# Optimization experiments

Hardware: AMD Instinct MI355X
Metric: run time of the kernel (lower is better)

Reference implementation:

```python
import jax, jax.numpy as jnp
import numpy as np

N_POINTS = 50000   # rows of features, also number of output segments
N_EDGES = 1600000  # ragged neighborhood edges (out_idx, in_idx)
CHANNELS = 64


def setup_inputs() -> dict:
    key = jax.random.key(0)
    k1, k2 = jax.random.split(key)
    features = jax.random.normal(k1, (N_POINTS, CHANNELS), dtype=jnp.float32)
    sparse_indices = jax.random.randint(
        k2, (N_EDGES, 2), 0, N_POINTS, dtype=jnp.int64
    )
    return {"features": features, "sparse_indices": sparse_indices}


def reference(features, sparse_indices):
    # sparse_indices[:, 0] = output segment id, sparse_indices[:, 1] = input row.
    out_idx = sparse_indices[:, 0]
    in_idx = sparse_indices[:, 1]
    gathered = features[in_idx]  # [E, C] gather of neighbor features
    # Unsorted segment max over the ragged neighborhoods -> [N, C].
    pooled = jax.ops.segment_max(gathered, out_idx, num_segments=N_POINTS)
    return pooled
```

## Files before the change

### kernel.cpp

```cpp
#include <hip/hip_runtime.h>
#include <hip/hip_bf16.h>
#include <math.h>


#define N_POINTS 50000
#define N_EDGES  1600000
#define CHANNELS 64
#define BIN_SHIFT 7
#define BIN_PTS   128
#define NBINS     391
#define NBINS_PAD 512
#define CAPB      5120
#define QCAP      1536
#define ECHUNK    4096
#define N_P1_BLOCKS ((N_EDGES + ECHUNK - 1) / ECHUNK)
#define GCUR_STRIDE 16
#define CVT_TOTAL (N_POINTS * CHANNELS / 4)
#define CVT_PER   2047

__device__ __forceinline__ unsigned int encode_bf16(float x) {
    unsigned int u = __float_as_uint(x);
    unsigned int r = ((u >> 16) & 1u) + 0x7FFFu;
    unsigned int h = (u + r) >> 16;
    return (h & 0x8000u) ? (h ^ 0xFFFFu) : (h | 0x8000u);
}

__device__ __forceinline__ float decode_u16(unsigned int v) {
    if (v == 0u) return -INFINITY;
    unsigned int h = (v & 0x8000u) ? (v ^ 0x8000u) : (v ^ 0xFFFFu);
    return __uint_as_float(h << 16);
}

__global__ __launch_bounds__(512) void binsort_cvt_kernel(
    const int2*   __restrict__ idx,
    const float4* __restrict__ feat4,
    uint2*        __restrict__ f16o,
    unsigned int* __restrict__ gcur,
    unsigned int* __restrict__ gstage)
{
    __shared__ unsigned int hist[NBINS_PAD];
    __shared__ unsigned int pfx[NBINS_PAD];
    __shared__ unsigned int gbase[NBINS_PAD];
    __shared__ unsigned int staging[ECHUNK];
    __shared__ unsigned int wsum[8];

    int tid  = threadIdx.x;
    int lane = tid & 63, w = tid >> 6;

    {
        int base = blockIdx.x * CVT_PER;
        #pragma unroll
        for (int k = 0; k < 4; ++k) {
            int i = base + k * 512 + tid;
            if (i < base + CVT_PER && i < CVT_TOTAL) {
                float4 v = feat4[i];
                uint2 r;
                r.x = encode_bf16(v.x) | (encode_bf16(v.y) << 16);
                r.y = encode_bf16(v.z) | (encode_bf16(v.w) << 16);
                f16o[i] = r;
            }
        }
    }

    int base = blockIdx.x * ECHUNK;
    int cnt  = N_EDGES - base; if (cnt > ECHUNK) cnt = ECHUNK;

    if (tid < NBINS_PAD) hist[tid] = 0u;
    __syncthreads();

    int2 e[8]; unsigned int slot[8];
    #pragma unroll
    for (int j = 0; j < 8; ++j) {
        int i = j * 512 + tid;
        if (i < cnt) {
            e[j] = idx[base + i];
            slot[j] = atomicAdd(&hist[(unsigned)e[j].x >> BIN_SHIFT], 1u);
        }
    }
    __syncthreads();

    unsigned int a = (tid < NBINS_PAD) ? hist[tid] : 0u;
    unsigned int inc = a;
    #pragma unroll
    for (int d = 1; d < 64; d <<= 1) {
        unsigned int v = __shfl_up(inc, d, 64);
        if (lane >= d) inc += v;
    }
    if (lane == 63) wsum[w] = inc;
    __syncthreads();
    unsigned int woff = 0;
    #pragma unroll
    for (int k = 0; k < 8; ++k) if (k < w) woff += wsum[k];
    if (tid < NBINS_PAD) {
        pfx[tid] = woff + inc - a;
        if (a) gbase[tid] = atomicAdd(&gcur[tid * GCUR_STRIDE], a);
    }
    __syncthreads();

    #pragma unroll
    for (int j = 0; j < 8; ++j) {
        int i = j * 512 + tid;
        if (i < cnt) {
            unsigned int dst = (unsigned)e[j].x, src = (unsigned)e[j].y;
            unsigned int bin = dst >> BIN_SHIFT;
            staging[pfx[bin] + slot[j]] =
                (bin << 23) | ((dst & (BIN_PTS - 1)) << 16) | src;
        }
    }
    __syncthreads();

    for (int i = tid; i < cnt; i += 512) {
        unsigned int v   = staging[i];
        unsigned int bin = v >> 23;
        unsigned int g   = gbase[bin] + ((unsigned)i - pfx[bin]);
        if (g < CAPB) gstage[(size_t)bin * CAPB + g] = v;
    }
}

__global__ __launch_bounds__(256) void pool_kernel(
    const unsigned int* __restrict__ feat16,
    const unsigned int* __restrict__ gcur,
    const unsigned int* __restrict__ gstage,
    float2* __restrict__ out2)
{
    __shared__ unsigned int sorted[QCAP];
    __shared__ unsigned int hist[32];
    __shared__ unsigned int start[33];
    __shared__ unsigned int cur[32];

    int tid = threadIdx.x;
    int bin = blockIdx.x >> 2;
    int quarter = blockIdx.x & 3;

    unsigned int cnt = gcur[bin * GCUR_STRIDE]; if (cnt > CAPB) cnt = CAPB;
    const uint4* list4 = (const uint4*)(gstage + (size_t)bin * CAPB);

    if (tid < 32) hist[tid] = 0u;
    __syncthreads();

    unsigned int e[16]; int ne = 0;
    for (unsigned int b4 = tid; b4 * 4 < cnt; b4 += 256) {
        uint4 v = list4[b4];
        unsigned int bi = b4 * 4;
        unsigned int vv[4] = {v.x, v.y, v.z, v.w};
        #pragma unroll
        for (int k = 0; k < 4; ++k) {
            if (bi + k < cnt) {
                unsigned int dl = (vv[k] >> 16) & (BIN_PTS - 1);
                if ((int)(dl >> 5) == quarter) {
                    e[ne++] = vv[k];
                    atomicAdd(&hist[dl & 31], 1u);
                }
            }
        }
    }
    __syncthreads();

    if (tid < 32) {
        unsigned int h = hist[tid], inc = h;
        #pragma unroll
        for (int d = 1; d < 32; d <<= 1) {
            unsigned int v = __shfl_up(inc, d, 64);
            if (tid >= d) inc += v;
        }
        start[tid] = inc - h; cur[tid] = inc - h;
        if (tid == 31) start[32] = inc;
    }
    __syncthreads();

    for (int j = 0; j < ne; ++j) {
        unsigned int v = e[j];
        unsigned int slot = atomicAdd(&cur[(v >> 16) & 31], 1u);
        if (slot < QCAP) sorted[slot] = v;
    }
    __syncthreads();

    int hw = tid >> 5, c2 = tid & 31;
    for (int p = hw; p < 32; p += 8) {
        unsigned int s0 = start[p], s1 = start[p + 1];
        if (s1 > QCAP) s1 = QCAP;
        unsigned int A0=0,A1=0,B0=0,B1=0,C0=0,C1=0,D0=0,D1=0;
        unsigned int E0=0,E1=0,F0=0,F1=0,G0=0,G1=0,H0=0,H1=0;
        unsigned int i = s0;
        for (; i + 8 <= s1; i += 8) {
            unsigned int u0 = feat16[(sorted[i+0] & 0xFFFFu) * 32 + c2];
            unsigned int u1 = feat16[(sorted[i+1] & 0xFFFFu) * 32 + c2];
            unsigned int u2 = feat16[(sorted[i+2] & 0xFFFFu) * 32 + c2];
            unsigned int u3 = feat16[(sorted[i+3] & 0xFFFFu) * 32 + c2];
            unsigned int u4 = feat16[(sorted[i+4] & 0xFFFFu) * 32 + c2];
            unsigned int u5 = feat16[(sorted[i+5] & 0xFFFFu) * 32 + c2];
            unsigned int u6 = feat16[(sorted[i+6] & 0xFFFFu) * 32 + c2];
            unsigned int u7 = feat16[(sorted[i+7] & 0xFFFFu) * 32 + c2];
            A0 = max(A0, u0 & 0xFFFFu); A1 = max(A1, u0 >> 16);
            B0 = max(B0, u1 & 0xFFFFu); B1 = max(B1, u1 >> 16);
            C0 = max(C0, u2 & 0xFFFFu); C1 = max(C1, u2 >> 16);
            D0 = max(D0, u3 & 0xFFFFu); D1 = max(D1, u3 >> 16);
            E0 = max(E0, u4 & 0xFFFFu); E1 = max(E1, u4 >> 16);
            F0 = max(F0, u5 & 0xFFFFu); F1 = max(F1, u5 >> 16);
            G0 = max(G0, u6 & 0xFFFFu); G1 = max(G1, u6 >> 16);
            H0 = max(H0, u7 & 0xFFFFu); H1 = max(H1, u7 >> 16);
        }
        for (; i < s1; ++i) {
            unsigned int u = feat16[(sorted[i] & 0xFFFFu) * 32 + c2];
            A0 = max(A0, u & 0xFFFFu); A1 = max(A1, u >> 16);
        }
        A0 = max(max(max(A0,B0), max(C0,D0)), max(max(E0,F0), max(G0,H0)));
        A1 = max(max(max(A1,B1), max(C1,D1)), max(max(E1,F1), max(G1,H1)));

        int gp = bin * BIN_PTS + quarter * 32 + p;
        if (gp < N_POINTS) {
            float2 f; f.x = decode_u16(A0); f.y = decode_u16(A1);
            out2[(size_t)gp * 32 + c2] = f;
        }
    }
}

extern "C" void kernel_launch(void* const* d_in, const int* in_sizes, int n_in,
                              void* d_out, int out_size, void* d_ws, size_t ws_size,
                              hipStream_t stream) {
    const float4* feat4 = (const float4*)d_in[0];
    const int2*   idx   = (const int2*)d_in[1];

    size_t off_gcur   = 0;
    size_t off_feat16 = (size_t)NBINS_PAD * GCUR_STRIDE * 4;
    size_t off_gstage = off_feat16 + (size_t)N_POINTS * CHANNELS * 2;
    unsigned int* gcur   = (unsigned int*)((char*)d_ws + off_gcur);
    uint2*        f16o   = (uint2*)((char*)d_ws + off_feat16);
    unsigned int* feat16 = (unsigned int*)((char*)d_ws + off_feat16);
    unsigned int* gstage = (unsigned int*)((char*)d_ws + off_gstage);

    hipMemsetAsync(gcur, 0, off_feat16, stream);
    binsort_cvt_kernel<<<N_P1_BLOCKS, 512, 0, stream>>>(idx, feat4, f16o, gcur, gstage);
    pool_kernel<<<NBINS * 4, 256, 0, stream>>>(feat16, gcur, gstage, (float2*)d_out);
}
```

Measured before the change: 122.6 us.

## Fuse memset, bin-sort and pooling into one cooperative persistent kernel

The memset, the bin-sort/convert kernel and the pooling kernel are merged into one cooperative kernel launched with a fixed grid of 512 blocks of 512 threads. Each block zeroes its own slice of the bin counters, and two grid-wide syncs separate the convert, bin-sort and pool phases. The pooling phase becomes a persistent loop over bin-quarter tasks and reuses the staging shared buffer as its sorted list. This is meant to remove two extra launches and the memset, at the cost of grid-sync latency and uneven task counts per block in the pool phase (about three tasks per block).

Result: slower. 452.8 us (+269.4%).

```diff
diff --git a/kernel.cpp b/kernel.cpp
--- a/kernel.cpp
+++ b/kernel.cpp
@@ -1,6 +1,8 @@
 #include <hip/hip_runtime.h>
-#include <hip/hip_bf16.h>
+#include <hip/hip_cooperative_groups.h>
 #include <math.h>
+
+namespace cg = cooperative_groups;
 
 
 #define N_POINTS 50000
@@ -11,12 +13,12 @@
 #define NBINS     391
 #define NBINS_PAD 512
 #define CAPB      5120
-#define QCAP      1536
-#define ECHUNK    4096
-#define N_P1_BLOCKS ((N_EDGES + ECHUNK - 1) / ECHUNK)
+#define GRID      512
+#define BLK       512
+#define ECHUNK    (N_EDGES / GRID)
 #define GCUR_STRIDE 16
 #define CVT_TOTAL (N_POINTS * CHANNELS / 4)
-#define CVT_PER   2047
+#define CVT_PER   ((CVT_TOTAL + GRID - 1) / GRID)
 
 __device__ __forceinline__ unsigned int encode_bf16(float x) {
     unsigned int u = __float_as_uint(x);
@@ -31,186 +33,183 @@
     return __uint_as_float(h << 16);
 }
 
-__global__ __launch_bounds__(512) void binsort_cvt_kernel(
+__global__ __launch_bounds__(BLK, 4) void fused_kernel(
     const int2*   __restrict__ idx,
     const float4* __restrict__ feat4,
-    uint2*        __restrict__ f16o,
-    unsigned int* __restrict__ gcur,
-    unsigned int* __restrict__ gstage)
+    unsigned int* feat16,
+    unsigned int* gcur,
+    unsigned int* gstage,
+    float2*       __restrict__ out2)
 {
+    __shared__ unsigned int staging[ECHUNK];
     __shared__ unsigned int hist[NBINS_PAD];
     __shared__ unsigned int pfx[NBINS_PAD];
     __shared__ unsigned int gbase[NBINS_PAD];
-    __shared__ unsigned int staging[ECHUNK];
     __shared__ unsigned int wsum[8];
-
-    int tid  = threadIdx.x;
-    int lane = tid & 63, w = tid >> 6;
-
+    __shared__ unsigned int qstart[33];
+    __shared__ unsigned int qcur[32];
+
+    cg::grid_group grid = cg::this_grid();
+    int tid = threadIdx.x, lane = tid & 63, w = tid >> 6;
+    int bid = blockIdx.x;
+
+    if (tid < GCUR_STRIDE) gcur[bid * GCUR_STRIDE + tid] = 0u;
     {
-        int base = blockIdx.x * CVT_PER;
+        int cb = bid * CVT_PER;
         #pragma unroll
         for (int k = 0; k < 4; ++k) {
-            int i = base + k * 512 + tid;
-            if (i < base + CVT_PER && i < CVT_TOTAL) {
+            int i = cb + k * BLK + tid;
+            if (i < cb + CVT_PER && i < CVT_TOTAL) {
                 float4 v = feat4[i];
                 uint2 r;
                 r.x = encode_bf16(v.x) | (encode_bf16(v.y) << 16);
                 r.y = encode_bf16(v.z) | (encode_bf16(v.w) << 16);
-                f16o[i] = r;
+                ((uint2*)feat16)[i] = r;
             }
         }
     }
-
-    int base = blockIdx.x * ECHUNK;
-    int cnt  = N_EDGES - base; if (cnt > ECHUNK) cnt = ECHUNK;
-
-    if (tid < NBINS_PAD) hist[tid] = 0u;
-    __syncthreads();
-
-    int2 e[8]; unsigned int slot[8];
-    #pragma unroll
-    for (int j = 0; j < 8; ++j) {
-        int i = j * 512 + tid;
-        if (i < cnt) {
-            e[j] = idx[base + i];
-            slot[j] = atomicAdd(&hist[(unsigned)e[j].x >> BIN_SHIFT], 1u);
-        }
-    }
-    __syncthreads();
-
-    unsigned int a = (tid < NBINS_PAD) ? hist[tid] : 0u;
-    unsigned int inc = a;
-    #pragma unroll
-    for (int d = 1; d < 64; d <<= 1) {
-        unsigned int v = __shfl_up(inc, d, 64);
-        if (lane >= d) inc += v;
-    }
-    if (lane == 63) wsum[w] = inc;
-    __syncthreads();
-    unsigned int woff = 0;
-    #pragma unroll
-    for (int k = 0; k < 8; ++k) if (k < w) woff += wsum[k];
-    if (tid < NBINS_PAD) {
+    __threadfence();
+    grid.sync();
+
+    {
+        int base = bid * ECHUNK;
+        hist[tid] = 0u;
+        __syncthreads();
+
+        int2 e[7]; unsigned int slot[7];
+        #pragma unroll
+        for (int j = 0; j < 7; ++j) {
+            int i = j * BLK + tid;
+            if (i < ECHUNK) {
+                e[j] = idx[base + i];
+                slot[j] = atomicAdd(&hist[(unsigned)e[j].x >> BIN_SHIFT], 1u);
+            }
+        }
+        __syncthreads();
+
+        unsigned int a = hist[tid];
+        unsigned int inc = a;
+        #pragma unroll
+        for (int d = 1; d < 64; d <<= 1) {
+            unsigned int v = __shfl_up(inc, d, 64);
+            if (lane >= d) inc += v;
+        }
+        if (lane == 63) wsum[w] = inc;
+        __syncthreads();
+        unsigned int woff = 0;
+        #pragma unroll
+        for (int k = 0; k < 8; ++k) if (k < w) woff += wsum[k];
         pfx[tid] = woff + inc - a;
         if (a) gbase[tid] = atomicAdd(&gcur[tid * GCUR_STRIDE], a);
+        __syncthreads();
+
+        #pragma unroll
+        for (int j = 0; j < 7; ++j) {
+            int i = j * BLK + tid;
+            if (i < ECHUNK) {
+                unsigned int dst = (unsigned)e[j].x, src = (unsigned)e[j].y;
+                unsigned int bin = dst >> BIN_SHIFT;
+                staging[pfx[bin] + slot[j]] =
+                    (bin << 23) | ((dst & (BIN_PTS - 1)) << 16) | src;
+            }
+        }
+        __syncthreads();
+
+        for (int i = tid; i < ECHUNK; i += BLK) {
+            unsigned int v   = staging[i];
+            unsigned int bin = v >> 23;
+            unsigned int g   = gbase[bin] + ((unsigned)i - pfx[bin]);
+            if (g < CAPB) gstage[(size_t)bin * CAPB + g] = v;
+        }
     }
-    __syncthreads();
-
-    #pragma unroll
-    for (int j = 0; j < 8; ++j) {
-        int i = j * 512 + tid;
-        if (i < cnt) {
-            unsigned int dst = (unsigned)e[j].x, src = (unsigned)e[j].y;
-            unsigned int bin = dst >> BIN_SHIFT;
-            staging[pfx[bin] + slot[j]] =
-                (bin << 23) | ((dst & (BIN_PTS - 1)) << 16) | src;
-        }
-    }
-    __syncthreads();
-
-    for (int i = tid; i < cnt; i += 512) {
-        unsigned int v   = staging[i];
-        unsigned int bin = v >> 23;
-        unsigned int g   = gbase[bin] + ((unsigned)i - pfx[bin]);
-        if (g < CAPB) gstage[(size_t)bin * CAPB + g] = v;
-    }
-}
-
-__global__ __launch_bounds__(256) void pool_kernel(
-    const unsigned int* __restrict__ feat16,
-    const unsigned int* __restrict__ gcur,
-    const unsigned int* __restrict__ gstage,
-    float2* __restrict__ out2)
-{
-    __shared__ unsigned int sorted[QCAP];
-    __shared__ unsigned int hist[32];
-    __shared__ unsigned int start[33];
-    __shared__ unsigned int cur[32];
-
-    int tid = threadIdx.x;
-    int bin = blockIdx.x >> 2;
-    int quarter = blockIdx.x & 3;
-
-    unsigned int cnt = gcur[bin * GCUR_STRIDE]; if (cnt > CAPB) cnt = CAPB;
-    const uint4* list4 = (const uint4*)(gstage + (size_t)bin * CAPB);
-
-    if (tid < 32) hist[tid] = 0u;
-    __syncthreads();
-
-    unsigned int e[16]; int ne = 0;
-    for (unsigned int b4 = tid; b4 * 4 < cnt; b4 += 256) {
-        uint4 v = list4[b4];
-        unsigned int bi = b4 * 4;
-        unsigned int vv[4] = {v.x, v.y, v.z, v.w};
-        #pragma unroll
-        for (int k = 0; k < 4; ++k) {
-            if (bi + k < cnt) {
-                unsigned int dl = (vv[k] >> 16) & (BIN_PTS - 1);
-                if ((int)(dl >> 5) == quarter) {
-                    e[ne++] = vv[k];
-                    atomicAdd(&hist[dl & 31], 1u);
+    __threadfence();
+    grid.sync();
+
+    for (int task = bid; task < NBINS * 4; task += GRID) {
+        int bin = task >> 2;
+        int quarter = task & 3;
+
+        __syncthreads();
+        if (tid < 32) hist[tid] = 0u;
+        __syncthreads();
+
+        unsigned int cnt = gcur[bin * GCUR_STRIDE]; if (cnt > CAPB) cnt = CAPB;
+        const uint4* list4 = (const uint4*)(gstage + (size_t)bin * CAPB);
+
+        unsigned int e[12]; int ne = 0;
+        for (unsigned int b4 = tid; b4 * 4 < cnt; b4 += BLK) {
+            uint4 v = list4[b4];
+            unsigned int bi = b4 * 4;
+            unsigned int vv[4] = {v.x, v.y, v.z, v.w};
+            #pragma unroll
+            for (int k = 0; k < 4; ++k) {
+                if (bi + k < cnt) {
+                    unsigned int dl = (vv[k] >> 16) & (BIN_PTS - 1);
+                    if ((int)(dl >> 5) == quarter) {
+                        e[ne++] = vv[k];
+                        atomicAdd(&hist[dl & 31], 1u);
+                    }
                 }
             }
         }
-    }
-    __syncthreads();
-
-    if (tid < 32) {
-        unsigned int h = hist[tid], inc = h;
-        #pragma unroll
-        for (int d = 1; d < 32; d <<= 1) {
-            unsigned int v = __shfl_up(inc, d, 64);
-            if (tid >= d) inc += v;
-        }
-        start[tid] = inc - h; cur[tid] = inc - h;
-        if (tid == 31) start[32] = inc;
-    }
-    __syncthreads();
-
-    for (int j = 0; j < ne; ++j) {
-        unsigned int v = e[j];
-        unsigned int slot = atomicAdd(&cur[(v >> 16) & 31], 1u);
-        if (slot < QCAP) sorted[slot] = v;
-    }
-    __syncthreads();
-
-    int hw = tid >> 5, c2 = tid & 31;
-    for (int p = hw; p < 32; p += 8) {
-        unsigned int s0 = start[p], s1 = start[p + 1];
-        if (s1 > QCAP) s1 = QCAP;
-        unsigned int A0=0,A1=0,B0=0,B1=0,C0=0,C1=0,D0=0,D1=0;
-        unsigned int E0=0,E1=0,F0=0,F1=0,G0=0,G1=0,H0=0,H1=0;
-        unsigned int i = s0;
-        for (; i + 8 <= s1; i += 8) {
-            unsigned int u0 = feat16[(sorted[i+0] & 0xFFFFu) * 32 + c2];
-            unsigned int u1 = feat16[(sorted[i+1] & 0xFFFFu) * 32 + c2];
-            unsigned int u2 = feat16[(sorted[i+2] & 0xFFFFu) * 32 + c2];
-            unsigned int u3 = feat16[(sorted[i+3] & 0xFFFFu) * 32 + c2];
-            unsigned int u4 = feat16[(sorted[i+4] & 0xFFFFu) * 32 + c2];
-            unsigned int u5 = feat16[(sorted[i+5] & 0xFFFFu) * 32 + c2];
-            unsigned int u6 = feat16[(sorted[i+6] & 0xFFFFu) * 32 + c2];
-            unsigned int u7 = feat16[(sorted[i+7] & 0xFFFFu) * 32 + c2];
-            A0 = max(A0, u0 & 0xFFFFu); A1 = max(A1, u0 >> 16);
-            B0 = max(B0, u1 & 0xFFFFu); B1 = max(B1, u1 >> 16);
-            C0 = max(C0, u2 & 0xFFFFu); C1 = max(C1, u2 >> 16);
-            D0 = max(D0, u3 & 0xFFFFu); D1 = max(D1, u3 >> 16);
-            E0 = max(E0, u4 & 0xFFFFu); E1 = max(E1, u4 >> 16);
-            F0 = max(F0, u5 & 0xFFFFu); F1 = max(F1, u5 >> 16);
-            G0 = max(G0, u6 & 0xFFFFu); G1 = max(G1, u6 >> 16);
-            H0 = max(H0, u7 & 0xFFFFu); H1 = max(H1, u7 >> 16);
-        }
-        for (; i < s1; ++i) {
-            unsigned int u = feat16[(sorted[i] & 0xFFFFu) * 32 + c2];
-            A0 = max(A0, u & 0xFFFFu); A1 = max(A1, u >> 16);
-        }
-        A0 = max(max(max(A0,B0), max(C0,D0)), max(max(E0,F0), max(G0,H0)));
-        A1 = max(max(max(A1,B1), max(C1,D1)), max(max(E1,F1), max(G1,H1)));
-
-        int gp = bin * BIN_PTS + quarter * 32 + p;
-        if (gp < N_POINTS) {
-            float2 f; f.x = decode_u16(A0); f.y = decode_u16(A1);
-            out2[(size_t)gp * 32 + c2] = f;
+        __syncthreads();
+
+        if (tid < 32) {
+            unsigned int h = hist[tid], inc = h;
+            #pragma unroll
+            for (int d = 1; d < 32; d <<= 1) {
+                unsigned int v = __shfl_up(inc, d, 64);
+                if (tid >= d) inc += v;
+            }
+            qstart[tid] = inc - h; qcur[tid] = inc - h;
+            if (tid == 31) qstart[32] = inc;
+        }
+        __syncthreads();
+
+        for (int j = 0; j < ne; ++j) {
+            unsigned int v = e[j];
+            unsigned int slot = atomicAdd(&qcur[(v >> 16) & 31], 1u);
+            if (slot < ECHUNK) staging[slot] = v;
+        }
+        __syncthreads();
+
+        int hw = tid >> 5, c2 = tid & 31;
+        for (int p = hw; p < 32; p += 16) {
+            unsigned int s0 = qstart[p], s1 = qstart[p + 1];
+            if (s1 > ECHUNK) s1 = ECHUNK;
+            unsigned int A0=0,A1=0,B0=0,B1=0,C0=0,C1=0,D0=0,D1=0;
+            unsigned int E0=0,E1=0,F0=0,F1=0,G0=0,G1=0,H0=0,H1=0;
+            unsigned int i = s0;
+            for (; i + 8 <= s1; i += 8) {
+                unsigned int u0 = feat16[(staging[i+0] & 0xFFFFu) * 32 + c2];
+                unsigned int u1 = feat16[(staging[i+1] & 0xFFFFu) * 32 + c2];
+                unsigned int u2 = feat16[(staging[i+2] & 0xFFFFu) * 32 + c2];
+                unsigned int u3 = feat16[(staging[i+3] & 0xFFFFu) * 32 + c2];
+                unsigned int u4 = feat16[(staging[i+4] & 0xFFFFu) * 32 + c2];
+                unsigned int u5 = feat16[(staging[i+5] & 0xFFFFu) * 32 + c2];
+                unsigned int u6 = feat16[(staging[i+6] & 0xFFFFu) * 32 + c2];
+                unsigned int u7 = feat16[(staging[i+7] & 0xFFFFu) * 32 + c2];
+                A0 = max(A0, u0 & 0xFFFFu); A1 = max(A1, u0 >> 16);
+                B0 = max(B0, u1 & 0xFFFFu); B1 = max(B1, u1 >> 16);
+                C0 = max(C0, u2 & 0xFFFFu); C1 = max(C1, u2 >> 16);
+                D0 = max(D0, u3 & 0xFFFFu); D1 = max(D1, u3 >> 16);
+                E0 = max(E0, u4 & 0xFFFFu); E1 = max(E1, u4 >> 16);
+                F0 = max(F0, u5 & 0xFFFFu); F1 = max(F1, u5 >> 16);
+                G0 = max(G0, u6 & 0xFFFFu); G1 = max(G1, u6 >> 16);
+                H0 = max(H0, u7 & 0xFFFFu); H1 = max(H1, u7 >> 16);
+            }
+            for (; i < s1; ++i) {
+                unsigned int u = feat16[(staging[i] & 0xFFFFu) * 32 + c2];
+                A0 = max(A0, u & 0xFFFFu); A1 = max(A1, u >> 16);
+            }
+            A0 = max(max(max(A0,B0), max(C0,D0)), max(max(E0,F0), max(G0,H0)));
+            A1 = max(max(max(A1,B1), max(C1,D1)), max(max(E1,F1), max(G1,H1)));
+
+            int gp = bin * BIN_PTS + quarter * 32 + p;
+            if (gp < N_POINTS) {
+                float2 f; f.x = decode_u16(A0); f.y = decode_u16(A1);
+                out2[(size_t)gp * 32 + c2] = f;
+            }
         }
     }
 }
@@ -220,16 +219,17 @@
                               hipStream_t stream) {
     const float4* feat4 = (const float4*)d_in[0];
     const int2*   idx   = (const int2*)d_in[1];
+    float2*       out2  = (float2*)d_out;
 
     size_t off_gcur   = 0;
     size_t off_feat16 = (size_t)NBINS_PAD * GCUR_STRIDE * 4;
     size_t off_gstage = off_feat16 + (size_t)N_POINTS * CHANNELS * 2;
     unsigned int* gcur   = (unsigned int*)((char*)d_ws + off_gcur);
-    uint2*        f16o   = (uint2*)((char*)d_ws + off_feat16);
     unsigned int* feat16 = (unsigned int*)((char*)d_ws + off_feat16);
     unsigned int* gstage = (unsigned int*)((char*)d_ws + off_gstage);
 
-    hipMemsetAsync(gcur, 0, off_feat16, stream);
-    binsort_cvt_kernel<<<N_P1_BLOCKS, 512, 0, stream>>>(idx, feat4, f16o, gcur, gstage);
-    pool_kernel<<<NBINS * 4, 256, 0, stream>>>(feat16, gcur, gstage, (float2*)d_out);
-}
+    void* args[] = { (void*)&idx, (void*)&feat4, (void*)&feat16,
+                     (void*)&gcur, (void*)&gstage, (void*)&out2 };
+    hipLaunchCooperativeKernel((void*)fused_kernel, dim3(GRID), dim3(BLK),
+                               args, 0, stream);
+}
```
